# Kernel tuning notes

Measured on AMD Instinct MI355X. Metric: run time of the kernel, lower is better.

## Reference

```python
import jax, jax.numpy as jnp
import numpy as np

V, E, T, H, NT, B = 30000, 300, 256, 256, 9, 128


def setup_inputs() -> dict:
    key = jax.random.key(0)
    ks = jax.random.split(key, 12)
    s = 0.05
    # token ids with trailing zero padding (0 = pad), lens in [T//2, T]
    lens = jax.random.randint(ks[0], (B,), T // 2, T + 1)
    tokens = jax.random.randint(ks[1], (B, T), 1, V)
    pos = jnp.arange(T)[None, :]
    inputs = jnp.where(pos < lens[:, None], tokens, 0)
    labels = jax.random.randint(ks[2], (B, T), 0, NT)
    emb = jax.random.normal(ks[3], (V, E), jnp.float32) * s
    Wf = jax.random.normal(ks[4], (E, 4 * H), jnp.float32) * s
    Uf = jax.random.normal(ks[5], (H, 4 * H), jnp.float32) * s
    bf = jnp.zeros((4 * H,), jnp.float32)
    Wb = jax.random.normal(ks[6], (E, 4 * H), jnp.float32) * s
    Ub = jax.random.normal(ks[7], (H, 4 * H), jnp.float32) * s
    bb = jnp.zeros((4 * H,), jnp.float32)
    fcW = jax.random.normal(ks[8], (2 * H, NT), jnp.float32) * s
    fcb = jnp.zeros((NT,), jnp.float32)
    trans = jax.random.uniform(ks[9], (NT, NT), jnp.float32)  # tf.random.uniform init
    return dict(inputs=inputs, labels=labels, emb=emb, Wf=Wf, Uf=Uf, bf=bf,
                Wb=Wb, Ub=Ub, bb=bb, fcW=fcW, fcb=fcb, trans=trans)


def _lstm(x, W, U, b):
    """Keras LSTM (gate order i,f,g,o). x: [B,T,E] -> [B,T,H]."""
    xW = jnp.einsum('bte,eh->bth', x, W) + b  # precompute input projections

    def step(carry, xt):
        h, c = carry
        z = xt + h @ U
        i, f, g, o = jnp.split(z, 4, axis=-1)
        i = jax.nn.sigmoid(i)
        f = jax.nn.sigmoid(f)
        g = jnp.tanh(g)
        o = jax.nn.sigmoid(o)
        c = f * c + i * g
        h = o * jnp.tanh(c)
        return (h, c), h

    Bq = x.shape[0]
    Hq = U.shape[0]
    init = (jnp.zeros((Bq, Hq), x.dtype), jnp.zeros((Bq, Hq), x.dtype))
    _, hs = jax.lax.scan(step, init, jnp.swapaxes(xW, 0, 1))  # [T,B,H]
    return jnp.swapaxes(hs, 0, 1)


def _crf_log_likelihood(logits, labels, lens, trans):
    """tfa.text.crf_log_likelihood: gold score - log partition. logits: [B,T,N]."""
    Bq, Tq, Nq = logits.shape
    pos = jnp.arange(Tq)[None, :]
    mask = pos < lens[:, None]  # [B,T]
    # unary (emission) score of the gold path
    unary = jnp.take_along_axis(logits, labels[..., None], axis=-1)[..., 0]
    score = jnp.sum(jnp.where(mask, unary, 0.0), axis=-1)
    # binary (transition) score of the gold path
    btrans = trans[labels[:, :-1], labels[:, 1:]]
    bmask = pos[:, 1:] < lens[:, None]
    score = score + jnp.sum(jnp.where(bmask, btrans, 0.0), axis=-1)
    # forward algorithm (log partition) with per-timestep length masking
    def step(alpha, inp):
        logit_t, m_t = inp  # [B,N], [B]
        new = jax.nn.logsumexp(alpha[:, :, None] + trans[None], axis=1) + logit_t
        return jnp.where(m_t[:, None], new, alpha), None

    alpha0 = logits[:, 0]
    xs = (jnp.swapaxes(logits[:, 1:], 0, 1), jnp.swapaxes(mask[:, 1:], 0, 1))
    alpha, _ = jax.lax.scan(step, alpha0, xs)
    log_norm = jax.nn.logsumexp(alpha, axis=-1)
    return score - log_norm


def reference(inputs, labels, emb, Wf, Uf, bf, Wb, Ub, bb, fcW, fcb, trans):
    text_lens = jnp.sum((inputs != 0).astype(jnp.int32), axis=-1)
    x = emb[inputs]  # [B,T,E]
    hf = _lstm(x, Wf, Uf, bf)
    hb = _lstm(x[:, ::-1], Wb, Ub, bb)[:, ::-1]
    h = jnp.concatenate([hf, hb], axis=-1)  # [B,T,2H]
    logits = h @ fcW + fcb  # [B,T,NT]
    log_likelihood = _crf_log_likelihood(logits, labels, text_lens, trans)
    return logits, log_likelihood, text_lens
```

## Files before the change

kernel.cpp:

```cpp
#include <hip/hip_runtime.h>
#include <hip/hip_bf16.h>
#include <stdint.h>

#define Bb 128
#define Tt 256
#define Ee 300
#define EP 320
#define Hh 256
#define G4 1024
#define NTAG 9

typedef __bf16 bf16x8 __attribute__((ext_vector_type(8)));
typedef float f32x4 __attribute__((ext_vector_type(4)));
typedef float f32x2 __attribute__((ext_vector_type(2)));
typedef int i32x8 __attribute__((ext_vector_type(8)));
typedef unsigned short u16;
typedef unsigned int u32;
typedef unsigned char u8;
typedef long i64;

union U4B { uint4 q; bf16x8 v; };

static __device__ __forceinline__ float bf2f(u32 u){
  union { float f; u32 u; } w; w.u = u << 16; return w.f;
}
static __device__ __forceinline__ u16 f2bf(float f){
  union { float f; u32 u; } w; w.f = f;
  u32 x = w.u;
  return (u16)((x + 0x7fffu + ((x >> 16) & 1u)) >> 16);
}
static __device__ __forceinline__ int perm2orig(int c){
  int w = c >> 7, r = c & 127, g = r >> 5, jj = r & 31;
  return g * 256 + w * 32 + jj;
}
static __device__ __forceinline__ float frcp(float x){ return __builtin_amdgcn_rcpf(x); }
static __device__ __forceinline__ float fexp2(float x){
  float r; asm("v_exp_f32 %0, %1" : "=v"(r) : "v"(x)); return r;
}
static __device__ __forceinline__ f32x2 vexp2(f32x2 x){
  f32x2 r; r[0] = fexp2(x[0]); r[1] = fexp2(x[1]); return r;
}
static __device__ __forceinline__ f32x2 vrcp(f32x2 x){
  f32x2 r; r[0] = frcp(x[0]); r[1] = frcp(x[1]); return r;
}
static __device__ __forceinline__ f32x2 vfabs(f32x2 x){
  f32x2 r; r[0] = __builtin_fabsf(x[0]); r[1] = __builtin_fabsf(x[1]); return r;
}
static __device__ __forceinline__ f32x2 vminc(f32x2 x, float c){
  f32x2 r; r[0] = fminf(x[0], c); r[1] = fminf(x[1], c); return r;
}
static __device__ __forceinline__ f32x2 vcps(f32x2 m, f32x2 s){
  f32x2 r; r[0] = __builtin_copysignf(m[0], s[0]);
  r[1] = __builtin_copysignf(m[1], s[1]); return r;
}
static __device__ __forceinline__ void gl_lds16(const void* g, void* l){
  __builtin_amdgcn_global_load_lds((const __attribute__((address_space(1))) u32*)(g),
                                   (__attribute__((address_space(3))) u32*)(l), 16, 0, 0);
}

__global__ void pack_w_k(const float* __restrict__ Wf, const float* __restrict__ Wb,
                         u16* __restrict__ Wpk){
  int idx = blockIdx.x * 256 + threadIdx.x;
  if(idx >= 128 * 10 * 64) return;
  int lane = idx & 63;
  int kk = (idx >> 6) % 10;
  int nt2 = idx / 640;
  int d = nt2 >> 6, ntd = nt2 & 63;
  int oc = perm2orig(ntd * 16 + (lane & 15));
  const float* W = d ? Wb : Wf;
  int k0 = kk * 32 + ((lane >> 4) << 3);
  u16 o[8];
  #pragma unroll
  for(int j = 0; j < 8; ++j){
    int k = k0 + j;
    o[j] = (k < Ee) ? f2bf(W[(size_t)k * G4 + oc]) : (u16)0;
  }
  uint4 q;
  q.x = o[0] | ((u32)o[1] << 16); q.y = o[2] | ((u32)o[3] << 16);
  q.z = o[4] | ((u32)o[5] << 16); q.w = o[6] | ((u32)o[7] << 16);
  *(uint4*)(Wpk + (size_t)idx * 8) = q;
}

__global__ void pack_u_k(const float* __restrict__ Uf, const float* __restrict__ Ub,
                         u8* __restrict__ Upk8){
  int idx = blockIdx.x * 256 + threadIdx.x;
  if(idx >= 2 * 64 * 2 * 64) return;
  int lane = idx & 63;
  int kh = (idx >> 6) & 1;
  int nt = (idx >> 7) & 63;
  int d = idx >> 13;
  int oc = perm2orig(nt * 16 + (lane & 15));
  const float* U = d ? Ub : Uf;
  int k0 = kh * 128 + (lane >> 4) * 32;
  u32 o[8];
  #pragma unroll
  for(int m = 0; m < 8; ++m){
    float v0 = U[(size_t)(k0 + 4 * m + 0) * G4 + oc] * 32.f;
    float v1 = U[(size_t)(k0 + 4 * m + 1) * G4 + oc] * 32.f;
    float v2 = U[(size_t)(k0 + 4 * m + 2) * G4 + oc] * 32.f;
    float v3 = U[(size_t)(k0 + 4 * m + 3) * G4 + oc] * 32.f;
    int pk = __builtin_amdgcn_cvt_pk_fp8_f32(v0, v1, 0, false);
    pk = __builtin_amdgcn_cvt_pk_fp8_f32(v2, v3, pk, true);
    o[m] = (u32)pk;
  }
  uint4* dst = (uint4*)(Upk8 + (size_t)idx * 32);
  dst[0] = (uint4){o[0], o[1], o[2], o[3]};
  dst[1] = (uint4){o[4], o[5], o[6], o[7]};
}

__global__ void pack_b_k(const float* __restrict__ bf_, const float* __restrict__ bb_,
                         float* __restrict__ bperm){
  int c = blockIdx.x * 256 + threadIdx.x;
  if(c >= 2048) return;
  const float* src = (c >> 10) ? bb_ : bf_;
  bperm[c] = src[perm2orig(c & 1023)];
}

__global__ void pack_fcw_k(const float* __restrict__ fcW, u8* __restrict__ fcw8){
  int idx = blockIdx.x * 256 + threadIdx.x;
  if(idx >= 1024) return;
  int lane = idx & 63, kk = idx >> 6;
  int col = lane & 15;
  int k0 = kk * 32 + ((lane >> 4) << 3);
  float v[8];
  #pragma unroll
  for(int j = 0; j < 8; ++j)
    v[j] = (col < NTAG) ? fcW[(size_t)(k0 + j) * NTAG + col] * 256.f : 0.f;
  int lo = __builtin_amdgcn_cvt_pk_fp8_f32(v[0], v[1], 0, false);
  lo = __builtin_amdgcn_cvt_pk_fp8_f32(v[2], v[3], lo, true);
  int hi = __builtin_amdgcn_cvt_pk_fp8_f32(v[4], v[5], 0, false);
  hi = __builtin_amdgcn_cvt_pk_fp8_f32(v[6], v[7], hi, true);
  uint2 q; q.x = (u32)lo; q.y = (u32)hi;
  *(uint2*)(fcw8 + (size_t)idx * 8) = q;
}

__global__ void gather_x_k(const int* __restrict__ inp, const float* __restrict__ emb,
                           u16* __restrict__ xbf){
  int row = blockIdx.x;
  int t = row >> 7, b = row & 127;
  int tok = inp[b * Tt + t];
  const float* src = emb + (size_t)tok * Ee;
  for(int e = threadIdx.x; e < EP; e += 64)
    xbf[(size_t)row * EP + e] = (e < Ee) ? f2bf(src[e]) : (u16)0;
}

__global__ __launch_bounds__(256, 2) void xw_gemm_k(const u16* __restrict__ xbf,
    const u16* __restrict__ Wpk, const float* __restrict__ bperm,
    u16* __restrict__ xwpk){
  __shared__ uint4 At[512];
  int t = blockIdx.y, nblk = blockIdx.x;
  int tid = threadIdx.x, lane = tid & 63, w = tid >> 6;
  int mh = w >> 1, nh = w & 1;
  f32x4 acc[4][4];
  #pragma unroll
  for(int i = 0; i < 4; ++i)
    #pragma unroll
    for(int j = 0; j < 4; ++j) acc[i][j] = (f32x4){0.f, 0.f, 0.f, 0.f};
  for(int ks = 0; ks < 10; ++ks){
    __syncthreads();
    #pragma unroll
    for(int it = 0; it < 2; ++it){
      int s = it * 256 + tid;
      int row = s >> 2, seg = s & 3;
      uint4 v = *(const uint4*)(xbf + (size_t)(t * 128 + row) * EP + ks * 32 + seg * 8);
      At[row * 4 + (seg ^ (row & 3))] = v;
    }
    __syncthreads();
    U4B a[4], bv[4];
    #pragma unroll
    for(int m = 0; m < 4; ++m){
      int row = (mh * 4 + m) * 16 + (lane & 15);
      a[m].q = At[row * 4 + ((lane >> 4) ^ (row & 3))];
    }
    #pragma unroll
    for(int n = 0; n < 4; ++n){
      int ntg = nblk * 8 + nh * 4 + n;
      bv[n].q = *(const uint4*)(Wpk + ((size_t)(ntg * 10 + ks) * 64 + lane) * 8);
    }
    #pragma unroll
    for(int m = 0; m < 4; ++m)
      #pragma unroll
      for(int n = 0; n < 4; ++n)
        acc[m][n] = __builtin_amdgcn_mfma_f32_16x16x32_bf16(a[m].v, bv[n].v, acc[m][n], 0, 0, 0);
  }
  #pragma unroll
  for(int m = 0; m < 4; ++m){
    int grp = mh * 4 + m;
    #pragma unroll
    for(int n = 0; n < 4; ++n){
      int ntg = nblk * 8 + nh * 4 + n;
      int d = ntg >> 6, nd = ntg & 63;
      float bias = bperm[ntg * 16 + (lane & 15)];
      u16 h0 = f2bf((acc[m][n][0] + bias) * 512.f), h1 = f2bf((acc[m][n][1] + bias) * 512.f);
      u16 h2 = f2bf((acc[m][n][2] + bias) * 512.f), h3 = f2bf((acc[m][n][3] + bias) * 512.f);
      uint2 p; p.x = h0 | ((u32)h1 << 16); p.y = h2 | ((u32)h3 << 16);
      *(uint2*)(xwpk + ((((size_t)(d * 8 + grp) * Tt + t) * 64 + nd) * 64 + lane) * 4) = p;
    }
  }
}

__global__ __launch_bounds__(512, 2) void lstm_rec_k(const u16* __restrict__ xwpk,
    const u8* __restrict__ Upk8, u8* __restrict__ hseq8){
  __shared__ u32 Hf8[2][1024];
  __shared__ uint2 Xw[2][4096];
  int bid = blockIdx.x;
  int d = bid >> 3, grp = bid & 7;
  int tid = threadIdx.x, lane = tid & 63, w = tid >> 6;
  int arow = lane & 15, r4 = lane >> 4;

  i32x8 Ureg[8][2];
  const u8* Ub8 = Upk8 + (size_t)d * 262144;
  #pragma unroll
  for(int n = 0; n < 8; ++n)
    #pragma unroll
    for(int kh = 0; kh < 2; ++kh)
      Ureg[n][kh] = *(const i32x8*)(Ub8 + (((size_t)(w * 8 + n) * 2 + kh) * 64 + lane) * 32);
  #pragma unroll
  for(int n = 0; n < 8; ++n)
    #pragma unroll
    for(int kh = 0; kh < 2; ++kh)
      asm volatile("" : "+a"(Ureg[n][kh]));

  Hf8[0][tid] = 0u; Hf8[0][tid + 512] = 0u;
  f32x2 cst2[2][2];
  #pragma unroll
  for(int a = 0; a < 2; ++a)
    #pragma unroll
    for(int p = 0; p < 2; ++p) cst2[a][p] = (f32x2){0.f, 0.f};
  const u16* xwb = xwpk + (size_t)(d * 8 + grp) * Tt * 16384;
  u8* hs_base = hseq8 + (size_t)(d * 8 + grp) * Tt * 4096;
  u32 hf8base = (u32)(uintptr_t)(&Hf8[0][0]);

  const float c1s = -1.44269504f / 512.f;
  const f32x2 C1  = (f32x2){c1s, c1s};
  const f32x2 C2  = (f32x2){2.f * c1s, 2.f * c1s};
  const f32x2 C3  = (f32x2){-2.f * 1.44269504f, -2.f * 1.44269504f};
  const f32x2 ONE = (f32x2){1.f, 1.f};

  {
    int t0 = d ? (Tt - 1) : 0;
    const u16* xwt0 = xwb + (size_t)t0 * 16384;
    #pragma unroll
    for(int j = 0; j < 4; ++j)
      gl_lds16(xwt0 + (w * 8 + 2 * j) * 256 + lane * 8, &Xw[0][w * 512 + 2 * j * 64]);
  }
  asm volatile("s_waitcnt vmcnt(0)" ::: "memory");
  __syncthreads();

  int cur = 0;
  for(int st = 0; st < Tt; ++st){
    int t = d ? (Tt - 1 - st) : st;
    int p = st & 1, c_ = p ^ 1;
    union AFU { i64 dd[4]; i32x8 v; };
    AFU af0, af1;
    u32 av = hf8base + (u32)(p * 4096) + (u32)(r4 * 512 + arow * 8);
    asm volatile("ds_read_b64_tr_b8 %0, %1"             : "=v"(af0.dd[0]) : "v"(av));
    asm volatile("ds_read_b64_tr_b8 %0, %1 offset:128"  : "=v"(af0.dd[1]) : "v"(av));
    asm volatile("ds_read_b64_tr_b8 %0, %1 offset:256"  : "=v"(af0.dd[2]) : "v"(av));
    asm volatile("ds_read_b64_tr_b8 %0, %1 offset:384"  : "=v"(af0.dd[3]) : "v"(av));
    asm volatile("ds_read_b64_tr_b8 %0, %1 offset:2048" : "=v"(af1.dd[0]) : "v"(av));
    asm volatile("ds_read_b64_tr_b8 %0, %1 offset:2176" : "=v"(af1.dd[1]) : "v"(av));
    asm volatile("ds_read_b64_tr_b8 %0, %1 offset:2304" : "=v"(af1.dd[2]) : "v"(av));
    asm volatile("ds_read_b64_tr_b8 %0, %1 offset:2432" : "=v"(af1.dd[3]) : "v"(av));
    asm volatile("s_waitcnt lgkmcnt(0)" ::: "memory");
    __builtin_amdgcn_sched_barrier(0);
    asm volatile("s_waitcnt vmcnt(2)" ::: "memory");
    uint2 xw[8];
    #pragma unroll
    for(int n = 0; n < 8; ++n) xw[n] = Xw[cur][w * 512 + n * 64 + lane];
    {
      int stn = (st + 1 < Tt) ? st + 1 : st;
      int tn = d ? (Tt - 1 - stn) : stn;
      const u16* xwtn = xwb + (size_t)tn * 16384;
      #pragma unroll
      for(int j = 0; j < 4; ++j)
        gl_lds16(xwtn + (w * 8 + 2 * j) * 256 + lane * 8, &Xw[cur ^ 1][w * 512 + 2 * j * 64]);
    }
    __builtin_amdgcn_sched_barrier(0);
    f32x4 acc[8];
    #pragma unroll
    for(int n = 0; n < 8; ++n){
      acc[n][0] = bf2f(xw[n].x & 0xffffu);
      acc[n][1] = bf2f(xw[n].x >> 16);
      acc[n][2] = bf2f(xw[n].y & 0xffffu);
      acc[n][3] = bf2f(xw[n].y >> 16);
    }
    #pragma unroll
    for(int n = 0; n < 8; ++n){
      asm volatile("v_mfma_f32_16x16x128_f8f6f4 %0, %1, %2, %0"
                   : "+v"(acc[n]) : "v"(af0.v), "a"(Ureg[n][0]));
      asm volatile("v_mfma_f32_16x16x128_f8f6f4 %0, %1, %2, %0"
                   : "+v"(acc[n]) : "v"(af1.v), "a"(Ureg[n][1]));
    }
    #pragma unroll
    for(int n1 = 0; n1 < 2; ++n1){
      f32x2 h16[2];
      #pragma unroll
      for(int pq = 0; pq < 2; ++pq){
        f32x2 ai = (f32x2){acc[0 + n1][2 * pq], acc[0 + n1][2 * pq + 1]};
        f32x2 af = (f32x2){acc[2 + n1][2 * pq], acc[2 + n1][2 * pq + 1]};
        f32x2 ag = (f32x2){acc[4 + n1][2 * pq], acc[4 + n1][2 * pq + 1]};
        f32x2 ao = (f32x2){acc[6 + n1][2 * pq], acc[6 + n1][2 * pq + 1]};
        f32x2 ei = vexp2(ai * C1);
        f32x2 ef = vexp2(af * C1);
        f32x2 eo = vexp2(ao * C1);
        f32x2 eg = vexp2(vminc(vfabs(ag), 10240.f) * C2);
        f32x2 ig = vcps(ONE - eg, ag) * vrcp((ONE + ei) * (ONE + eg));
        f32x2 fs = vrcp(ONE + ef);
        f32x2 cc = fs * cst2[n1][pq] + ig;
        cst2[n1][pq] = cc;
        f32x2 ec = vexp2(vminc(vfabs(cc), 20.f) * C3);
        f32x2 hh = vcps(ONE - ec, cc) * vrcp((ONE + eo) * (ONE + ec));
        h16[pq] = hh * (f32x2){16.f, 16.f};
      }
      int pk = __builtin_amdgcn_cvt_pk_fp8_f32(h16[0][0], h16[0][1], 0, false);
      pk = __builtin_amdgcn_cvt_pk_fp8_f32(h16[1][0], h16[1][1], pk, true);
      int unit = w * 32 + n1 * 16 + arow;
      Hf8[c_][unit * 4 + r4] = (u32)pk;
      *(u32*)(hs_base + (size_t)t * 4096 + unit * 16 + r4 * 4) = (u32)pk;
    }
    asm volatile("s_waitcnt lgkmcnt(0)" ::: "memory");
    __builtin_amdgcn_s_barrier();
    cur ^= 1;
  }
}

__global__ __launch_bounds__(256) void logits_k(const u8* __restrict__ hseq8,
    const u8* __restrict__ fcw8, const float* __restrict__ fcb,
    float* __restrict__ out){
  __shared__ u8 Ht[4][8192];
  int widx = threadIdx.x >> 6, lane = threadIdx.x & 63;
  int wid = blockIdx.x * 4 + widx;
  int grp = wid >> 8, t = wid & 255;
  i64 bf[16];
  #pragma unroll
  for(int kk = 0; kk < 16; ++kk)
    bf[kk] = *(const i64*)(fcw8 + ((size_t)kk * 64 + lane) * 8);
  const u8* hf = hseq8 + ((size_t)(0 * 8 + grp) * Tt + t) * 4096;
  const u8* hb = hseq8 + ((size_t)(1 * 8 + grp) * Tt + t) * 4096;
  #pragma unroll
  for(int j = 0; j < 4; ++j){
    gl_lds16(hf + j * 1024 + lane * 16, &Ht[widx][j * 1024]);
    gl_lds16(hb + j * 1024 + lane * 16, &Ht[widx][4096 + j * 1024]);
  }
  asm volatile("s_waitcnt vmcnt(0)" ::: "memory");
  __builtin_amdgcn_sched_barrier(0);
  u32 base = (u32)(uintptr_t)(&Ht[widx][0]) + lane * 8;
  i64 afr[16];
  #pragma unroll
  for(int kk = 0; kk < 16; ++kk){
    u32 a = base + kk * 512;
    asm volatile("ds_read_b64_tr_b8 %0, %1" : "=v"(afr[kk]) : "v"(a));
  }
  asm volatile("s_waitcnt lgkmcnt(0)" ::: "memory");
  __builtin_amdgcn_sched_barrier(0);
  f32x4 acc = (f32x4){0.f, 0.f, 0.f, 0.f};
  #pragma unroll
  for(int kk = 0; kk < 16; ++kk)
    acc = __builtin_amdgcn_mfma_f32_16x16x32_fp8_fp8(afr[kk], bf[kk], acc, 0, 0, 0);
  int tag = lane & 15, r4 = lane >> 4;
  if(tag < NTAG){
    float bb = fcb[tag];
    #pragma unroll
    for(int q = 0; q < 4; ++q){
      int b = grp * 16 + r4 * 4 + q;
      out[((size_t)b * Tt + t) * NTAG + tag] = acc[q] * (1.f / 4096.f) + bb;
    }
  }
}

__global__ __launch_bounds__(64) void crf_k(const int* __restrict__ inp,
    const int* __restrict__ labels, const float* __restrict__ trans,
    const float* __restrict__ logits, float* __restrict__ out){
  int b = blockIdx.x;
  int lane = threadIdx.x;
  int cnt = 0;
  for(int t = lane; t < Tt; t += 64) cnt += (inp[b * Tt + t] != 0) ? 1 : 0;
  #pragma unroll
  for(int off = 32; off >= 1; off >>= 1) cnt += __shfl_xor(cnt, off, 64);
  int len = cnt;
  float sc = 0.f;
  for(int t = lane; t < Tt; t += 64){
    if(t < len){
      int lab = labels[b * Tt + t];
      sc += logits[(size_t)(b * Tt + t) * NTAG + lab];
      if(t >= 1){
        int lp = labels[b * Tt + t - 1];
        sc += trans[lp * NTAG + lab];
      }
    }
  }
  #pragma unroll
  for(int off = 32; off >= 1; off >>= 1) sc += __shfl_xor(sc, off, 64);
  float Tc[NTAG];
  if(lane < NTAG){
    #pragma unroll
    for(int i = 0; i < NTAG; ++i) Tc[i] = trans[i * NTAG + lane];
  }
  float alpha = (lane < NTAG) ? logits[(size_t)(b * Tt) * NTAG + lane] : -3.0e38f;
  for(int t = 1; t < len; ++t){
    float av[NTAG];
    #pragma unroll
    for(int i = 0; i < NTAG; ++i) av[i] = __shfl(alpha, i, 64);
    if(lane < NTAG){
      float m = av[0] + Tc[0];
      #pragma unroll
      for(int i = 1; i < NTAG; ++i) m = fmaxf(m, av[i] + Tc[i]);
      float s = 0.f;
      #pragma unroll
      for(int i = 0; i < NTAG; ++i) s += __expf(av[i] + Tc[i] - m);
      alpha = __logf(s) + m + logits[(size_t)(b * Tt + t) * NTAG + lane];
    }
  }
  float av[NTAG];
  #pragma unroll
  for(int i = 0; i < NTAG; ++i) av[i] = __shfl(alpha, i, 64);
  float m = av[0];
  #pragma unroll
  for(int i = 1; i < NTAG; ++i) m = fmaxf(m, av[i]);
  float s = 0.f;
  #pragma unroll
  for(int i = 0; i < NTAG; ++i) s += __expf(av[i] - m);
  float ln = __logf(s) + m;
  if(lane == 0){
    out[(size_t)Bb * Tt * NTAG + b] = sc - ln;
    out[(size_t)Bb * Tt * NTAG + Bb + b] = (float)len;
  }
}

extern "C" void kernel_launch(void* const* d_in, const int* in_sizes, int n_in,
                              void* d_out, int out_size, void* d_ws, size_t ws_size,
                              hipStream_t stream) {
  const int*   inputs = (const int*)d_in[0];
  const int*   labels = (const int*)d_in[1];
  const float* emb    = (const float*)d_in[2];
  const float* Wf     = (const float*)d_in[3];
  const float* Uf     = (const float*)d_in[4];
  const float* bf_    = (const float*)d_in[5];
  const float* Wb     = (const float*)d_in[6];
  const float* Ub     = (const float*)d_in[7];
  const float* bb_    = (const float*)d_in[8];
  const float* fcW    = (const float*)d_in[9];
  const float* fcb    = (const float*)d_in[10];
  const float* trans  = (const float*)d_in[11];
  float* out = (float*)d_out;
  char* ws = (char*)d_ws;
  u16*   xwpk  = (u16*)(ws + 0);
  u8*    hseq8 = (u8*) (ws + 134217728);
  u8*    Upk8  = (u8*) (ws + 150994944);
  u16*   Wpk   = (u16*)(ws + 151519232);
  float* bperm = (float*)(ws + 152829952);
  u8*    fcw8  = (u8*) (ws + 152838144);
  u16*   xbf   = (u16*)(ws + 152846336);

  hipLaunchKernelGGL(pack_w_k, dim3(320), dim3(256), 0, stream, Wf, Wb, Wpk);
  hipLaunchKernelGGL(pack_u_k, dim3(64), dim3(256), 0, stream, Uf, Ub, Upk8);
  hipLaunchKernelGGL(pack_b_k, dim3(8), dim3(256), 0, stream, bf_, bb_, bperm);
  hipLaunchKernelGGL(pack_fcw_k, dim3(4), dim3(256), 0, stream, fcW, fcw8);
  hipLaunchKernelGGL(gather_x_k, dim3(32768), dim3(64), 0, stream, inputs, emb, xbf);
  hipLaunchKernelGGL(xw_gemm_k, dim3(16, 256), dim3(256), 0, stream, xbf, Wpk, bperm, xwpk);
  hipLaunchKernelGGL(lstm_rec_k, dim3(16), dim3(512), 0, stream, xwpk, Upk8, hseq8);
  hipLaunchKernelGGL(logits_k, dim3(512), dim3(256), 0, stream, hseq8, fcw8, fcb, out);
  hipLaunchKernelGGL(crf_k, dim3(128), dim3(64), 0, stream, inputs, labels, trans, out, out);
}
```

Baseline: 579.7 us.

## Split LSTM recurrence across two blocks per group with global h exchange

Each (direction, batch-group) recurrence now runs on two workgroups instead of one. Each workgroup owns half of the hidden units and holds half of the U weights. At every step the two workgroups exchange their fp8 hidden-state halves through global memory, using atomic counters as a spin-wait handshake. The first MFMA on the workgroup's own half is issued before waiting on the partner's half, to overlap compute with the wait. This doubles the number of CUs working on the serial recurrence and halves per-CU MFMA and activation work per step, at the cost of a cross-CU global-memory synchronisation on every timestep.

```diff
diff --git a/kernel.cpp b/kernel.cpp
--- a/kernel.cpp
+++ b/kernel.cpp
@@ -30,8 +30,8 @@
   return (u16)((x + 0x7fffu + ((x >> 16) & 1u)) >> 16);
 }
 static __device__ __forceinline__ int perm2orig(int c){
-  int w = c >> 7, r = c & 127, g = r >> 5, jj = r & 31;
-  return g * 256 + w * 32 + jj;
+  int w16 = c >> 6, g = (c >> 4) & 3, j = c & 15;
+  return g * 256 + w16 * 16 + j;
 }
 static __device__ __forceinline__ float frcp(float x){ return __builtin_amdgcn_rcpf(x); }
 static __device__ __forceinline__ float fexp2(float x){
@@ -134,6 +134,10 @@
   *(uint2*)(fcw8 + (size_t)idx * 8) = q;
 }
 
+__global__ void zero_ctr_k(u32* __restrict__ ctrs){
+  if(threadIdx.x < 32) ctrs[threadIdx.x] = 0u;
+}
+
 __global__ void gather_x_k(const int* __restrict__ inp, const float* __restrict__ emb,
                            u16* __restrict__ xbf){
   int row = blockIdx.x;
@@ -200,36 +204,43 @@
 }
 
 __global__ __launch_bounds__(512, 2) void lstm_rec_k(const u16* __restrict__ xwpk,
-    const u8* __restrict__ Upk8, u8* __restrict__ hseq8){
+    const u8* __restrict__ Upk8, u8* __restrict__ hseq8,
+    u32* __restrict__ xch, u32* __restrict__ ctrs){
   __shared__ u32 Hf8[2][1024];
-  __shared__ uint2 Xw[2][4096];
+  __shared__ u8 XwB[2][16384];
   int bid = blockIdx.x;
-  int d = bid >> 3, grp = bid & 7;
+  int half = bid & 1, dg = bid >> 1;
+  int d = dg >> 3, grp = dg & 7;
   int tid = threadIdx.x, lane = tid & 63, w = tid >> 6;
   int arow = lane & 15, r4 = lane >> 4;
-
-  i32x8 Ureg[8][2];
+  int w16 = half * 8 + w;
+
+  i32x8 Ureg[4][2];
   const u8* Ub8 = Upk8 + (size_t)d * 262144;
   #pragma unroll
-  for(int n = 0; n < 8; ++n)
-    #pragma unroll
-    for(int kh = 0; kh < 2; ++kh)
-      Ureg[n][kh] = *(const i32x8*)(Ub8 + (((size_t)(w * 8 + n) * 2 + kh) * 64 + lane) * 32);
-  #pragma unroll
-  for(int n = 0; n < 8; ++n)
-    #pragma unroll
-    for(int kh = 0; kh < 2; ++kh)
-      asm volatile("" : "+a"(Ureg[n][kh]));
+  for(int n = 0; n < 4; ++n){
+    int ntd = w16 * 4 + n;
+    Ureg[n][0] = *(const i32x8*)(Ub8 + (((size_t)ntd * 2 + half) * 64 + lane) * 32);
+    Ureg[n][1] = *(const i32x8*)(Ub8 + (((size_t)ntd * 2 + (half ^ 1)) * 64 + lane) * 32);
+  }
+  #pragma unroll
+  for(int n = 0; n < 4; ++n){
+    asm volatile("" : "+a"(Ureg[n][0]));
+    asm volatile("" : "+a"(Ureg[n][1]));
+  }
 
   Hf8[0][tid] = 0u; Hf8[0][tid + 512] = 0u;
-  f32x2 cst2[2][2];
-  #pragma unroll
-  for(int a = 0; a < 2; ++a)
-    #pragma unroll
-    for(int p = 0; p < 2; ++p) cst2[a][p] = (f32x2){0.f, 0.f};
-  const u16* xwb = xwpk + (size_t)(d * 8 + grp) * Tt * 16384;
-  u8* hs_base = hseq8 + (size_t)(d * 8 + grp) * Tt * 4096;
+  f32x2 cst2[2];
+  cst2[0] = (f32x2){0.f, 0.f}; cst2[1] = (f32x2){0.f, 0.f};
+  const u16* xwb = xwpk + (size_t)dg * Tt * 16384;
+  u8* hs_base = hseq8 + (size_t)dg * Tt * 4096;
   u32 hf8base = (u32)(uintptr_t)(&Hf8[0][0]);
+  u32* hf8u = (u32*)(&Hf8[0][0]);
+  u32* myctr = ctrs + dg * 2 + half;
+  u32* pctr  = ctrs + dg * 2 + (half ^ 1);
+  u32 ownoff = (u32)(half * 2048), partoff = (u32)((half ^ 1) * 2048);
+  int partu = (half ^ 1) * 512;
+  int xidx = w * 64 + (lane & 15) * 4 + (lane >> 4);
 
   const float c1s = -1.44269504f / 512.f;
   const f32x2 C1  = (f32x2){c1s, c1s};
@@ -239,10 +250,9 @@
 
   {
     int t0 = d ? (Tt - 1) : 0;
-    const u16* xwt0 = xwb + (size_t)t0 * 16384;
-    #pragma unroll
-    for(int j = 0; j < 4; ++j)
-      gl_lds16(xwt0 + (w * 8 + 2 * j) * 256 + lane * 8, &Xw[0][w * 512 + 2 * j * 64]);
+    const u8* src = (const u8*)(xwb + (size_t)t0 * 16384) + half * 16384 + tid * 32;
+    gl_lds16(src, &XwB[0][tid * 32]);
+    gl_lds16(src + 16, &XwB[0][tid * 32 + 16]);
   }
   asm volatile("s_waitcnt vmcnt(0)" ::: "memory");
   __syncthreads();
@@ -251,75 +261,97 @@
   for(int st = 0; st < Tt; ++st){
     int t = d ? (Tt - 1 - st) : st;
     int p = st & 1, c_ = p ^ 1;
+    if(st && tid == 0)
+      __hip_atomic_fetch_add(myctr, 1u, __ATOMIC_RELAXED, __HIP_MEMORY_SCOPE_AGENT);
     union AFU { i64 dd[4]; i32x8 v; };
-    AFU af0, af1;
-    u32 av = hf8base + (u32)(p * 4096) + (u32)(r4 * 512 + arow * 8);
-    asm volatile("ds_read_b64_tr_b8 %0, %1"             : "=v"(af0.dd[0]) : "v"(av));
-    asm volatile("ds_read_b64_tr_b8 %0, %1 offset:128"  : "=v"(af0.dd[1]) : "v"(av));
-    asm volatile("ds_read_b64_tr_b8 %0, %1 offset:256"  : "=v"(af0.dd[2]) : "v"(av));
-    asm volatile("ds_read_b64_tr_b8 %0, %1 offset:384"  : "=v"(af0.dd[3]) : "v"(av));
-    asm volatile("ds_read_b64_tr_b8 %0, %1 offset:2048" : "=v"(af1.dd[0]) : "v"(av));
-    asm volatile("ds_read_b64_tr_b8 %0, %1 offset:2176" : "=v"(af1.dd[1]) : "v"(av));
-    asm volatile("ds_read_b64_tr_b8 %0, %1 offset:2304" : "=v"(af1.dd[2]) : "v"(av));
-    asm volatile("ds_read_b64_tr_b8 %0, %1 offset:2432" : "=v"(af1.dd[3]) : "v"(av));
+    AFU afo, afp;
+    u32 avo = hf8base + (u32)(p * 4096) + ownoff + (u32)(r4 * 512 + arow * 8);
+    asm volatile("ds_read_b64_tr_b8 %0, %1"            : "=v"(afo.dd[0]) : "v"(avo));
+    asm volatile("ds_read_b64_tr_b8 %0, %1 offset:128" : "=v"(afo.dd[1]) : "v"(avo));
+    asm volatile("ds_read_b64_tr_b8 %0, %1 offset:256" : "=v"(afo.dd[2]) : "v"(avo));
+    asm volatile("ds_read_b64_tr_b8 %0, %1 offset:384" : "=v"(afo.dd[3]) : "v"(avo));
     asm volatile("s_waitcnt lgkmcnt(0)" ::: "memory");
     __builtin_amdgcn_sched_barrier(0);
-    asm volatile("s_waitcnt vmcnt(2)" ::: "memory");
-    uint2 xw[8];
-    #pragma unroll
-    for(int n = 0; n < 8; ++n) xw[n] = Xw[cur][w * 512 + n * 64 + lane];
+    uint2 xw4[4];
+    #pragma unroll
+    for(int n = 0; n < 4; ++n)
+      xw4[n] = ((const uint2*)&XwB[cur][0])[(w * 4 + n) * 64 + lane];
     {
       int stn = (st + 1 < Tt) ? st + 1 : st;
       int tn = d ? (Tt - 1 - stn) : stn;
-      const u16* xwtn = xwb + (size_t)tn * 16384;
-      #pragma unroll
-      for(int j = 0; j < 4; ++j)
-        gl_lds16(xwtn + (w * 8 + 2 * j) * 256 + lane * 8, &Xw[cur ^ 1][w * 512 + 2 * j * 64]);
+      const u8* src = (const u8*)(xwb + (size_t)tn * 16384) + half * 16384 + tid * 32;
+      gl_lds16(src, &XwB[cur ^ 1][tid * 32]);
+      gl_lds16(src + 16, &XwB[cur ^ 1][tid * 32 + 16]);
     }
     __builtin_amdgcn_sched_barrier(0);
-    f32x4 acc[8];
-    #pragma unroll
-    for(int n = 0; n < 8; ++n){
-      acc[n][0] = bf2f(xw[n].x & 0xffffu);
-      acc[n][1] = bf2f(xw[n].x >> 16);
-      acc[n][2] = bf2f(xw[n].y & 0xffffu);
-      acc[n][3] = bf2f(xw[n].y >> 16);
-    }
-    #pragma unroll
-    for(int n = 0; n < 8; ++n){
+    f32x4 acc[4];
+    #pragma unroll
+    for(int n = 0; n < 4; ++n){
+      acc[n][0] = bf2f(xw4[n].x & 0xffffu);
+      acc[n][1] = bf2f(xw4[n].x >> 16);
+      acc[n][2] = bf2f(xw4[n].y & 0xffffu);
+      acc[n][3] = bf2f(xw4[n].y >> 16);
+    }
+    #pragma unroll
+    for(int n = 0; n < 4; ++n)
       asm volatile("v_mfma_f32_16x16x128_f8f6f4 %0, %1, %2, %0"
-                   : "+v"(acc[n]) : "v"(af0.v), "a"(Ureg[n][0]));
+                   : "+v"(acc[n]) : "v"(afo.v), "a"(Ureg[n][0]));
+    if(st){
+      u32 tgt = (u32)st;
+      if(lane == 0){
+        int guard = 0; u32 vv;
+        do {
+          vv = __hip_atomic_fetch_add(pctr, 0u, __ATOMIC_RELAXED, __HIP_MEMORY_SCOPE_AGENT);
+        } while(vv < tgt && ++guard < (1 << 20));
+      }
+      u32* pxch = xch + ((size_t)(dg * 2 + (p ^ 1)) * 2 + (half ^ 1)) * 512;
+      u32 v = __hip_atomic_fetch_add(&pxch[w * 64 + lane], 0u,
+                                     __ATOMIC_RELAXED, __HIP_MEMORY_SCOPE_AGENT);
+      hf8u[p * 1024 + partu + w * 64 + lane] = v;
+    }
+    asm volatile("s_waitcnt lgkmcnt(0)" ::: "memory");
+    __builtin_amdgcn_s_barrier();
+    u32 avp = hf8base + (u32)(p * 4096) + partoff + (u32)(r4 * 512 + arow * 8);
+    asm volatile("ds_read_b64_tr_b8 %0, %1"            : "=v"(afp.dd[0]) : "v"(avp));
+    asm volatile("ds_read_b64_tr_b8 %0, %1 offset:128" : "=v"(afp.dd[1]) : "v"(avp));
+    asm volatile("ds_read_b64_tr_b8 %0, %1 offset:256" : "=v"(afp.dd[2]) : "v"(avp));
+    asm volatile("ds_read_b64_tr_b8 %0, %1 offset:384" : "=v"(afp.dd[3]) : "v"(avp));
+    asm volatile("s_waitcnt lgkmcnt(0)" ::: "memory");
+    __builtin_amdgcn_sched_barrier(0);
+    #pragma unroll
+    for(int n = 0; n < 4; ++n)
       asm volatile("v_mfma_f32_16x16x128_f8f6f4 %0, %1, %2, %0"
-                   : "+v"(acc[n]) : "v"(af1.v), "a"(Ureg[n][1]));
-    }
-    #pragma unroll
-    for(int n1 = 0; n1 < 2; ++n1){
-      f32x2 h16[2];
-      #pragma unroll
-      for(int pq = 0; pq < 2; ++pq){
-        f32x2 ai = (f32x2){acc[0 + n1][2 * pq], acc[0 + n1][2 * pq + 1]};
-        f32x2 af = (f32x2){acc[2 + n1][2 * pq], acc[2 + n1][2 * pq + 1]};
-        f32x2 ag = (f32x2){acc[4 + n1][2 * pq], acc[4 + n1][2 * pq + 1]};
-        f32x2 ao = (f32x2){acc[6 + n1][2 * pq], acc[6 + n1][2 * pq + 1]};
-        f32x2 ei = vexp2(ai * C1);
-        f32x2 ef = vexp2(af * C1);
-        f32x2 eo = vexp2(ao * C1);
-        f32x2 eg = vexp2(vminc(vfabs(ag), 10240.f) * C2);
-        f32x2 ig = vcps(ONE - eg, ag) * vrcp((ONE + ei) * (ONE + eg));
-        f32x2 fs = vrcp(ONE + ef);
-        f32x2 cc = fs * cst2[n1][pq] + ig;
-        cst2[n1][pq] = cc;
-        f32x2 ec = vexp2(vminc(vfabs(cc), 20.f) * C3);
-        f32x2 hh = vcps(ONE - ec, cc) * vrcp((ONE + eo) * (ONE + ec));
-        h16[pq] = hh * (f32x2){16.f, 16.f};
-      }
-      int pk = __builtin_amdgcn_cvt_pk_fp8_f32(h16[0][0], h16[0][1], 0, false);
-      pk = __builtin_amdgcn_cvt_pk_fp8_f32(h16[1][0], h16[1][1], pk, true);
-      int unit = w * 32 + n1 * 16 + arow;
-      Hf8[c_][unit * 4 + r4] = (u32)pk;
-      *(u32*)(hs_base + (size_t)t * 4096 + unit * 16 + r4 * 4) = (u32)pk;
-    }
-    asm volatile("s_waitcnt lgkmcnt(0)" ::: "memory");
+                   : "+v"(acc[n]) : "v"(afp.v), "a"(Ureg[n][1]));
+    f32x2 h16[2];
+    #pragma unroll
+    for(int pq = 0; pq < 2; ++pq){
+      f32x2 ai = (f32x2){acc[0][2 * pq], acc[0][2 * pq + 1]};
+      f32x2 af = (f32x2){acc[1][2 * pq], acc[1][2 * pq + 1]};
+      f32x2 ag = (f32x2){acc[2][2 * pq], acc[2][2 * pq + 1]};
+      f32x2 ao = (f32x2){acc[3][2 * pq], acc[3][2 * pq + 1]};
+      f32x2 ei = vexp2(ai * C1);
+      f32x2 ef = vexp2(af * C1);
+      f32x2 eo = vexp2(ao * C1);
+      f32x2 eg = vexp2(vminc(vfabs(ag), 10240.f) * C2);
+      f32x2 ig = vcps(ONE - eg, ag) * vrcp((ONE + ei) * (ONE + eg));
+      f32x2 fs = vrcp(ONE + ef);
+      f32x2 cc = fs * cst2[pq] + ig;
+      cst2[pq] = cc;
+      f32x2 ec = vexp2(vminc(vfabs(cc), 20.f) * C3);
+      f32x2 hh = vcps(ONE - ec, cc) * vrcp((ONE + eo) * (ONE + ec));
+      h16[pq] = hh * (f32x2){16.f, 16.f};
+    }
+    int pk = __builtin_amdgcn_cvt_pk_fp8_f32(h16[0][0], h16[0][1], 0, false);
+    pk = __builtin_amdgcn_cvt_pk_fp8_f32(h16[1][0], h16[1][1], pk, true);
+    int unit = w16 * 16 + arow;
+    hf8u[c_ * 1024 + unit * 4 + r4] = (u32)pk;
+    *(u32*)(hs_base + (size_t)t * 4096 + unit * 16 + r4 * 4) = (u32)pk;
+    {
+      u32* myxch = xch + ((size_t)(dg * 2 + p) * 2 + half) * 512;
+      __hip_atomic_exchange(&myxch[xidx], (u32)pk,
+                            __ATOMIC_RELAXED, __HIP_MEMORY_SCOPE_AGENT);
+    }
+    asm volatile("s_waitcnt vmcnt(0) lgkmcnt(0)" ::: "memory");
     __builtin_amdgcn_s_barrier();
     cur ^= 1;
   }
@@ -452,14 +484,17 @@
   float* bperm = (float*)(ws + 152829952);
   u8*    fcw8  = (u8*) (ws + 152838144);
   u16*   xbf   = (u16*)(ws + 152846336);
+  u32*   xch   = (u32*)(ws + 173817856);
+  u32*   ctrs  = (u32*)(ws + 173948928);
 
   hipLaunchKernelGGL(pack_w_k, dim3(320), dim3(256), 0, stream, Wf, Wb, Wpk);
   hipLaunchKernelGGL(pack_u_k, dim3(64), dim3(256), 0, stream, Uf, Ub, Upk8);
   hipLaunchKernelGGL(pack_b_k, dim3(8), dim3(256), 0, stream, bf_, bb_, bperm);
   hipLaunchKernelGGL(pack_fcw_k, dim3(4), dim3(256), 0, stream, fcW, fcw8);
+  hipLaunchKernelGGL(zero_ctr_k, dim3(1), dim3(64), 0, stream, ctrs);
   hipLaunchKernelGGL(gather_x_k, dim3(32768), dim3(64), 0, stream, inputs, emb, xbf);
   hipLaunchKernelGGL(xw_gemm_k, dim3(16, 256), dim3(256), 0, stream, xbf, Wpk, bperm, xwpk);
-  hipLaunchKernelGGL(lstm_rec_k, dim3(16), dim3(512), 0, stream, xwpk, Upk8, hseq8);
+  hipLaunchKernelGGL(lstm_rec_k, dim3(32), dim3(512), 0, stream, xwpk, Upk8, hseq8, xch, ctrs);
   hipLaunchKernelGGL(logits_k, dim3(512), dim3(256), 0, stream, hseq8, fcw8, fcb, out);
   hipLaunchKernelGGL(crf_k, dim3(128), dim3(64), 0, stream, inputs, labels, trans, out, out);
 }
```

After: 807.2 us. 1.39x slower.

## Split LSTM recurrence across 16 waves per block with half the columns each

Applied to the files above, without the earlier changes.

Doubles the recurrent kernel's block size from 512 to 1024 threads, so each wave owns 4 gate column tiles (one 16-unit slice across i,f,g,o) instead of 8. The gate permutation, the staging of the input projection and the layout of the hidden-state writes are reworked to match. The aim is to shorten the serial per-timestep critical path: fewer MFMAs and less activation math per wave, and more waves to hide latency. In exchange, each step's barrier now spans twice as many waves and register pressure per CU rises.

```diff
diff --git a/kernel.cpp b/kernel.cpp
--- a/kernel.cpp
+++ b/kernel.cpp
@@ -30,8 +30,8 @@
   return (u16)((x + 0x7fffu + ((x >> 16) & 1u)) >> 16);
 }
 static __device__ __forceinline__ int perm2orig(int c){
-  int w = c >> 7, r = c & 127, g = r >> 5, jj = r & 31;
-  return g * 256 + w * 32 + jj;
+  int w16 = c >> 6, g = (c >> 4) & 3, j = c & 15;
+  return g * 256 + w16 * 16 + j;
 }
 static __device__ __forceinline__ float frcp(float x){ return __builtin_amdgcn_rcpf(x); }
 static __device__ __forceinline__ float fexp2(float x){
@@ -199,37 +199,35 @@
   }
 }
 
-__global__ __launch_bounds__(512, 2) void lstm_rec_k(const u16* __restrict__ xwpk,
+__global__ __launch_bounds__(1024, 4) void lstm_rec_k(const u16* __restrict__ xwpk,
     const u8* __restrict__ Upk8, u8* __restrict__ hseq8){
   __shared__ u32 Hf8[2][1024];
-  __shared__ uint2 Xw[2][4096];
+  __shared__ u8 XwB[2][32768];
   int bid = blockIdx.x;
   int d = bid >> 3, grp = bid & 7;
   int tid = threadIdx.x, lane = tid & 63, w = tid >> 6;
   int arow = lane & 15, r4 = lane >> 4;
 
-  i32x8 Ureg[8][2];
+  i32x8 Ureg[4][2];
   const u8* Ub8 = Upk8 + (size_t)d * 262144;
   #pragma unroll
-  for(int n = 0; n < 8; ++n)
+  for(int n = 0; n < 4; ++n)
     #pragma unroll
     for(int kh = 0; kh < 2; ++kh)
-      Ureg[n][kh] = *(const i32x8*)(Ub8 + (((size_t)(w * 8 + n) * 2 + kh) * 64 + lane) * 32);
-  #pragma unroll
-  for(int n = 0; n < 8; ++n)
-    #pragma unroll
-    for(int kh = 0; kh < 2; ++kh)
-      asm volatile("" : "+a"(Ureg[n][kh]));
-
-  Hf8[0][tid] = 0u; Hf8[0][tid + 512] = 0u;
-  f32x2 cst2[2][2];
-  #pragma unroll
-  for(int a = 0; a < 2; ++a)
-    #pragma unroll
-    for(int p = 0; p < 2; ++p) cst2[a][p] = (f32x2){0.f, 0.f};
+      Ureg[n][kh] = *(const i32x8*)(Ub8 + (((size_t)(w * 4 + n) * 2 + kh) * 64 + lane) * 32);
+  #pragma unroll
+  for(int n = 0; n < 4; ++n){
+    asm volatile("" : "+a"(Ureg[n][0]));
+    asm volatile("" : "+a"(Ureg[n][1]));
+  }
+
+  Hf8[0][tid & 1023] = 0u;
+  f32x2 cst2[2];
+  cst2[0] = (f32x2){0.f, 0.f}; cst2[1] = (f32x2){0.f, 0.f};
   const u16* xwb = xwpk + (size_t)(d * 8 + grp) * Tt * 16384;
   u8* hs_base = hseq8 + (size_t)(d * 8 + grp) * Tt * 4096;
   u32 hf8base = (u32)(uintptr_t)(&Hf8[0][0]);
+  u32* hf8u = (u32*)(&Hf8[0][0]);
 
   const float c1s = -1.44269504f / 512.f;
   const f32x2 C1  = (f32x2){c1s, c1s};
@@ -239,10 +237,9 @@
 
   {
     int t0 = d ? (Tt - 1) : 0;
-    const u16* xwt0 = xwb + (size_t)t0 * 16384;
-    #pragma unroll
-    for(int j = 0; j < 4; ++j)
-      gl_lds16(xwt0 + (w * 8 + 2 * j) * 256 + lane * 8, &Xw[0][w * 512 + 2 * j * 64]);
+    const u8* src = (const u8*)(xwb + (size_t)t0 * 16384) + w * 2048;
+    gl_lds16(src + lane * 16, &XwB[0][w * 2048]);
+    gl_lds16(src + 1024 + lane * 16, &XwB[0][w * 2048 + 1024]);
   }
   asm volatile("s_waitcnt vmcnt(0)" ::: "memory");
   __syncthreads();
@@ -264,61 +261,58 @@
     asm volatile("ds_read_b64_tr_b8 %0, %1 offset:2432" : "=v"(af1.dd[3]) : "v"(av));
     asm volatile("s_waitcnt lgkmcnt(0)" ::: "memory");
     __builtin_amdgcn_sched_barrier(0);
-    asm volatile("s_waitcnt vmcnt(2)" ::: "memory");
-    uint2 xw[8];
-    #pragma unroll
-    for(int n = 0; n < 8; ++n) xw[n] = Xw[cur][w * 512 + n * 64 + lane];
+    asm volatile("s_waitcnt vmcnt(1)" ::: "memory");
+    uint2 xw4[4];
+    #pragma unroll
+    for(int n = 0; n < 4; ++n)
+      xw4[n] = *(const uint2*)(&XwB[cur][w * 2048 + n * 512 + lane * 8]);
     {
       int stn = (st + 1 < Tt) ? st + 1 : st;
       int tn = d ? (Tt - 1 - stn) : stn;
-      const u16* xwtn = xwb + (size_t)tn * 16384;
-      #pragma unroll
-      for(int j = 0; j < 4; ++j)
-        gl_lds16(xwtn + (w * 8 + 2 * j) * 256 + lane * 8, &Xw[cur ^ 1][w * 512 + 2 * j * 64]);
+      const u8* src = (const u8*)(xwb + (size_t)tn * 16384) + w * 2048;
+      gl_lds16(src + lane * 16, &XwB[cur ^ 1][w * 2048]);
+      gl_lds16(src + 1024 + lane * 16, &XwB[cur ^ 1][w * 2048 + 1024]);
     }
     __builtin_amdgcn_sched_barrier(0);
-    f32x4 acc[8];
-    #pragma unroll
-    for(int n = 0; n < 8; ++n){
-      acc[n][0] = bf2f(xw[n].x & 0xffffu);
-      acc[n][1] = bf2f(xw[n].x >> 16);
-      acc[n][2] = bf2f(xw[n].y & 0xffffu);
-      acc[n][3] = bf2f(xw[n].y >> 16);
-    }
-    #pragma unroll
-    for(int n = 0; n < 8; ++n){
+    f32x4 acc[4];
+    #pragma unroll
+    for(int n = 0; n < 4; ++n){
+      acc[n][0] = bf2f(xw4[n].x & 0xffffu);
+      acc[n][1] = bf2f(xw4[n].x >> 16);
+      acc[n][2] = bf2f(xw4[n].y & 0xffffu);
+      acc[n][3] = bf2f(xw4[n].y >> 16);
+    }
+    #pragma unroll
+    for(int n = 0; n < 4; ++n){
       asm volatile("v_mfma_f32_16x16x128_f8f6f4 %0, %1, %2, %0"
                    : "+v"(acc[n]) : "v"(af0.v), "a"(Ureg[n][0]));
       asm volatile("v_mfma_f32_16x16x128_f8f6f4 %0, %1, %2, %0"
                    : "+v"(acc[n]) : "v"(af1.v), "a"(Ureg[n][1]));
     }
-    #pragma unroll
-    for(int n1 = 0; n1 < 2; ++n1){
-      f32x2 h16[2];
-      #pragma unroll
-      for(int pq = 0; pq < 2; ++pq){
-        f32x2 ai = (f32x2){acc[0 + n1][2 * pq], acc[0 + n1][2 * pq + 1]};
-        f32x2 af = (f32x2){acc[2 + n1][2 * pq], acc[2 + n1][2 * pq + 1]};
-        f32x2 ag = (f32x2){acc[4 + n1][2 * pq], acc[4 + n1][2 * pq + 1]};
-        f32x2 ao = (f32x2){acc[6 + n1][2 * pq], acc[6 + n1][2 * pq + 1]};
-        f32x2 ei = vexp2(ai * C1);
-        f32x2 ef = vexp2(af * C1);
-        f32x2 eo = vexp2(ao * C1);
-        f32x2 eg = vexp2(vminc(vfabs(ag), 10240.f) * C2);
-        f32x2 ig = vcps(ONE - eg, ag) * vrcp((ONE + ei) * (ONE + eg));
-        f32x2 fs = vrcp(ONE + ef);
-        f32x2 cc = fs * cst2[n1][pq] + ig;
-        cst2[n1][pq] = cc;
-        f32x2 ec = vexp2(vminc(vfabs(cc), 20.f) * C3);
-        f32x2 hh = vcps(ONE - ec, cc) * vrcp((ONE + eo) * (ONE + ec));
-        h16[pq] = hh * (f32x2){16.f, 16.f};
-      }
-      int pk = __builtin_amdgcn_cvt_pk_fp8_f32(h16[0][0], h16[0][1], 0, false);
-      pk = __builtin_amdgcn_cvt_pk_fp8_f32(h16[1][0], h16[1][1], pk, true);
-      int unit = w * 32 + n1 * 16 + arow;
-      Hf8[c_][unit * 4 + r4] = (u32)pk;
-      *(u32*)(hs_base + (size_t)t * 4096 + unit * 16 + r4 * 4) = (u32)pk;
-    }
+    f32x2 h16[2];
+    #pragma unroll
+    for(int pq = 0; pq < 2; ++pq){
+      f32x2 ai = (f32x2){acc[0][2 * pq], acc[0][2 * pq + 1]};
+      f32x2 af = (f32x2){acc[1][2 * pq], acc[1][2 * pq + 1]};
+      f32x2 ag = (f32x2){acc[2][2 * pq], acc[2][2 * pq + 1]};
+      f32x2 ao = (f32x2){acc[3][2 * pq], acc[3][2 * pq + 1]};
+      f32x2 ei = vexp2(ai * C1);
+      f32x2 ef = vexp2(af * C1);
+      f32x2 eo = vexp2(ao * C1);
+      f32x2 eg = vexp2(vminc(vfabs(ag), 10240.f) * C2);
+      f32x2 ig = vcps(ONE - eg, ag) * vrcp((ONE + ei) * (ONE + eg));
+      f32x2 fs = vrcp(ONE + ef);
+      f32x2 cc = fs * cst2[pq] + ig;
+      cst2[pq] = cc;
+      f32x2 ec = vexp2(vminc(vfabs(cc), 20.f) * C3);
+      f32x2 hh = vcps(ONE - ec, cc) * vrcp((ONE + eo) * (ONE + ec));
+      h16[pq] = hh * (f32x2){16.f, 16.f};
+    }
+    int pk = __builtin_amdgcn_cvt_pk_fp8_f32(h16[0][0], h16[0][1], 0, false);
+    pk = __builtin_amdgcn_cvt_pk_fp8_f32(h16[1][0], h16[1][1], pk, true);
+    int unit = w * 16 + arow;
+    hf8u[c_ * 1024 + unit * 4 + r4] = (u32)pk;
+    *(u32*)(hs_base + (size_t)t * 4096 + unit * 16 + r4 * 4) = (u32)pk;
     asm volatile("s_waitcnt lgkmcnt(0)" ::: "memory");
     __builtin_amdgcn_s_barrier();
     cur ^= 1;
@@ -459,7 +453,7 @@
   hipLaunchKernelGGL(pack_fcw_k, dim3(4), dim3(256), 0, stream, fcW, fcw8);
   hipLaunchKernelGGL(gather_x_k, dim3(32768), dim3(64), 0, stream, inputs, emb, xbf);
   hipLaunchKernelGGL(xw_gemm_k, dim3(16, 256), dim3(256), 0, stream, xbf, Wpk, bperm, xwpk);
-  hipLaunchKernelGGL(lstm_rec_k, dim3(16), dim3(512), 0, stream, xwpk, Upk8, hseq8);
+  hipLaunchKernelGGL(lstm_rec_k, dim3(16), dim3(1024), 0, stream, xwpk, Upk8, hseq8);
   hipLaunchKernelGGL(logits_k, dim3(512), dim3(256), 0, stream, hseq8, fcw8, fcb, out);
   hipLaunchKernelGGL(crf_k, dim3(128), dim3(64), 0, stream, inputs, labels, trans, out, out);
 }
```

New measurement: 580.6 us. No clear change (+0.1%).
